# Optimization experiments

Measured on AMD Instinct MI355X. Metric: run time of the kernel, lower is better.

## Reference

```python
import jax, jax.numpy as jnp
import numpy as np

D_IN = 1024
D_OUT = 1024
SEQ = 4096


def setup_inputs() -> dict:
    key = jax.random.key(0)
    kx, kq, kk, kv = jax.random.split(key, 4)
    x = jax.random.normal(kx, (SEQ, D_IN), dtype=jnp.float32)
    # torch.rand -> uniform [0,1)
    wquery = jax.random.uniform(kq, (D_IN, D_OUT), dtype=jnp.float32)
    wkey = jax.random.uniform(kk, (D_IN, D_OUT), dtype=jnp.float32)
    wvalue = jax.random.uniform(kv, (D_IN, D_OUT), dtype=jnp.float32)
    return {"x": x, "wquery": wquery, "wkey": wkey, "wvalue": wvalue}


def reference(x, wquery, wkey, wvalue):
    keys = x @ wkey          # [S, d_out]
    queries = x @ wquery     # [S, d_out]
    values = x @ wvalue      # [S, d_out]
    scale = 1.0 / jnp.sqrt(jnp.float32(keys.shape[-1]))
    attn_scores = queries @ keys.T            # [S, S]
    attn_weights = jax.nn.softmax(attn_scores * scale, axis=-1)
    context = attn_weights @ values           # [S, d_out]
    return context
```

## Files before the change

kernel.cpp:

```cpp
#include <hip/hip_runtime.h>
#include <math.h>

#define SEQ 4096
#define DIM 1024

typedef _Float16 f16;
typedef _Float16 f16x8 __attribute__((ext_vector_type(8)));
typedef _Float16 f16x4 __attribute__((ext_vector_type(4)));
typedef float f32x4 __attribute__((ext_vector_type(4)));

#define GLOAD_LDS16(g, l)                                              \
    __builtin_amdgcn_global_load_lds(                                  \
        (const __attribute__((address_space(1))) void*)(g),            \
        (__attribute__((address_space(3))) void*)(l), 16, 0, 0)

__global__ __launch_bounds__(256) void split16(const float* __restrict__ in,
                                               f16* __restrict__ hi,
                                               f16* __restrict__ lo, int n4) {
    const int i = blockIdx.x * 256 + threadIdx.x;
    if (i >= n4) return;
    const float4 v = ((const float4*)in)[i];
    const float vv[4] = {v.x, v.y, v.z, v.w};
    f16x4 h, l;
#pragma unroll
    for (int q = 0; q < 4; ++q) {
        const f16 hq = (f16)vv[q];
        h[q] = hq;
        l[q] = (f16)(vv[q] - (float)hq);
    }
    ((f16x4*)hi)[i] = h;
    ((f16x4*)lo)[i] = l;
}

__global__ __launch_bounds__(256) void wtrans3h(
    const float* __restrict__ Wq, const float* __restrict__ Wk,
    const float* __restrict__ Wv,
    f16* __restrict__ QT, f16* __restrict__ KT, f16* __restrict__ VT) {
    __shared__ float tile[32][33];
    const int tid = threadIdx.x;
    const int r0 = blockIdx.x * 32;
    const int c0 = blockIdx.y * 32;
    const int z = blockIdx.z;
    const float* W = (z == 0) ? Wq : (z == 1) ? Wk : Wv;
    f16* T = (z == 0) ? QT : (z == 1) ? KT : VT;
    const float off = (z < 2) ? 0.5f : 0.0f;
    {
        const int r = tid >> 3, c = (tid & 7) * 4;
        const float4 v = *(const float4*)&W[(size_t)(r0 + r) * DIM + c0 + c];
        tile[r][c + 0] = v.x;
        tile[r][c + 1] = v.y;
        tile[r][c + 2] = v.z;
        tile[r][c + 3] = v.w;
    }
    __syncthreads();
    {
        const int n = tid >> 3;
        const int k = (tid & 7) * 4;
        f16x4 h;
#pragma unroll
        for (int q = 0; q < 4; ++q) h[q] = (f16)(tile[k + q][n] - off);
        *(f16x4*)&T[(size_t)(c0 + n) * DIM + r0 + k] = h;
    }
}

__global__ __launch_bounds__(256) void rowsum_x(const float* __restrict__ X,
                                                float* __restrict__ sx) {
    const int row = blockIdx.x * 4 + (threadIdx.x >> 6);
    const int lane = threadIdx.x & 63;
    const float4* r4 = (const float4*)(X + (size_t)row * DIM);
    float s = 0.f;
#pragma unroll
    for (int c = 0; c < 4; ++c) {
        const float4 f = r4[lane + 64 * c];
        s += f.x + f.y + f.z + f.w;
    }
#pragma unroll
    for (int m = 32; m >= 1; m >>= 1) s += __shfl_xor(s, m);
    if (lane == 0) sx[row] = s;
}

__global__ __launch_bounds__(256) void rowsum_hl(
    const f16* __restrict__ Qh, const f16* __restrict__ Ql,
    const f16* __restrict__ Kh, const f16* __restrict__ Kl,
    float* __restrict__ rq, float* __restrict__ rk) {
    const f16 *H, *L;
    float* out;
    if (blockIdx.y == 0) { H = Qh; L = Ql; out = rq; }
    else                 { H = Kh; L = Kl; out = rk; }
    const int row = blockIdx.x * 4 + (threadIdx.x >> 6);
    const int lane = threadIdx.x & 63;
    const f16x8* h8 = (const f16x8*)(H + (size_t)row * DIM);
    const f16x8* l8 = (const f16x8*)(L + (size_t)row * DIM);
    float s = 0.f;
#pragma unroll
    for (int c = 0; c < 2; ++c) {
        const f16x8 a = h8[lane + 64 * c];
        const f16x8 b = l8[lane + 64 * c];
#pragma unroll
        for (int e = 0; e < 8; ++e) s += (float)a[e] + (float)b[e];
    }
#pragma unroll
    for (int m = 32; m >= 1; m >>= 1) s += __shfl_xor(s, m);
    if (lane == 0) out[row] = s;
}

#define EPI_F32 0
#define EPI_SPLIT16 1
#define EPI_TRANS16 2

template <int EPI, int NPAIR, int KTILES>
__global__ __launch_bounds__(256, 2) void gemm128h(
    const f16* __restrict__ A0, const f16* __restrict__ A1,
    const f16* __restrict__ B0a, const f16* __restrict__ B1a,
    const f16* __restrict__ B0b, const f16* __restrict__ B1b,
    int ysplit, int N, int ldA, int ldB, float scale,
    void* out0a, void* out1a, void* out0b, void* out1b) {
    __shared__ __align__(16) f16 As[2][128 * 64];
    __shared__ __align__(16) f16 Bs[2][128 * 64];

    const int tid = threadIdx.x;
    const int lane = tid & 63;
    const int wid = tid >> 6;
    const int wr = wid >> 1, wc = wid & 1;

    const int total = (int)(gridDim.y << 5);
    int lid = (int)blockIdx.y * 32 + (int)blockIdx.x;
    lid = (lid & 7) * (total >> 3) + (lid >> 3);
    const int bx = lid & 31;
    int by = lid >> 5;

    const f16 *B0, *B1;
    void *o0, *o1;
    if (by >= ysplit) {
        by -= ysplit;
        B0 = B0b; B1 = B1b;
        o0 = out0b; o1 = out1b;
    } else {
        B0 = B0a; B1 = B1a;
        o0 = out0a; o1 = out1a;
    }
    const int m0 = bx * 128;
    const int n0 = by * 128;

    const f16* APs[2] = {A0, A1};
    const f16* BPs[2] = {B0, B1};
    const int nt = NPAIR * KTILES;

    f32x4 acc[4][4];
#pragma unroll
    for (int i = 0; i < 4; ++i)
#pragma unroll
        for (int j = 0; j < 4; ++j) acc[i][j] = (f32x4){0.f, 0.f, 0.f, 0.f};

    auto STAGE = [&](int t, int b) {
        const int pass = t / KTILES;
        const int k0 = (t % KTILES) * 64;
        const f16* Ap = APs[pass];
        const f16* Bp = BPs[pass];
#pragma unroll
        for (int L = 0; L < 4; ++L) {
            const int idx = L * 256 + tid;
            const int row = idx >> 3;
            const int sc = ((idx & 7) * 16) ^ ((row & 7) << 4);
            const int ldsu = (L * 256 + (tid & ~63)) * 8;
            GLOAD_LDS16(Ap + (size_t)(m0 + row) * ldA + k0 + (sc >> 1),
                        &As[b][ldsu]);
            GLOAD_LDS16(Bp + (size_t)(n0 + row) * ldB + k0 + (sc >> 1),
                        &Bs[b][ldsu]);
        }
    };

    STAGE(0, 0);

    for (int t = 0; t < nt; ++t) {
        const int cur = t & 1;
        __builtin_amdgcn_s_barrier();
        asm volatile("" ::: "memory");
        if (t + 1 < nt) {
            STAGE(t + 1, cur ^ 1);
            asm volatile("s_waitcnt vmcnt(8)" ::: "memory");
        } else {
            asm volatile("s_waitcnt vmcnt(0)" ::: "memory");
        }
        __builtin_amdgcn_s_barrier();
        asm volatile("" ::: "memory");

#pragma unroll
        for (int kk = 0; kk < 2; ++kk) {
            const int cb = kk * 64 + (lane >> 4) * 16;
            f16x8 af[4], bv[4];
#pragma unroll
            for (int i = 0; i < 4; ++i) {
                const int r = wr * 64 + i * 16 + (lane & 15);
                af[i] = *(const f16x8*)(&As[cur][r * 64 +
                                                 ((cb ^ ((r & 7) << 4)) >> 1)]);
            }
#pragma unroll
            for (int j = 0; j < 4; ++j) {
                const int r = wc * 64 + j * 16 + (lane & 15);
                bv[j] = *(const f16x8*)(&Bs[cur][r * 64 +
                                                 ((cb ^ ((r & 7) << 4)) >> 1)]);
            }
            __builtin_amdgcn_s_setprio(1);
#pragma unroll
            for (int i = 0; i < 4; ++i)
#pragma unroll
                for (int j = 0; j < 4; ++j)
                    acc[i][j] = __builtin_amdgcn_mfma_f32_16x16x32_f16(
                        af[i], bv[j], acc[i][j], 0, 0, 0);
            __builtin_amdgcn_s_setprio(0);
        }
    }

    const int row0 = m0 + wr * 64 + (lane >> 4) * 4;
    const int col0 = n0 + wc * 64 + (lane & 15);

    if (EPI == EPI_F32) {
        float* O = (float*)o0;
#pragma unroll
        for (int i = 0; i < 4; ++i)
#pragma unroll
            for (int j = 0; j < 4; ++j)
#pragma unroll
                for (int q = 0; q < 4; ++q)
                    O[(size_t)(row0 + i * 16 + q) * N + col0 + j * 16] =
                        acc[i][j][q] * scale;
    } else if (EPI == EPI_SPLIT16) {
        f16* Hi = (f16*)o0;
        f16* Lo = (f16*)o1;
#pragma unroll
        for (int i = 0; i < 4; ++i)
#pragma unroll
            for (int j = 0; j < 4; ++j)
#pragma unroll
                for (int q = 0; q < 4; ++q) {
                    const float x = acc[i][j][q];
                    const f16 h = (f16)x;
                    const size_t idx = (size_t)(row0 + i * 16 + q) * N + col0 + j * 16;
                    Hi[idx] = h;
                    Lo[idx] = (f16)(x - (float)h);
                }
    } else {
        f16* OT = (f16*)o0;
#pragma unroll
        for (int i = 0; i < 4; ++i)
#pragma unroll
            for (int j = 0; j < 4; ++j) {
                f16x4 v;
#pragma unroll
                for (int q = 0; q < 4; ++q) v[q] = (f16)acc[i][j][q];
                *(f16x4*)&OT[(size_t)(col0 + j * 16) * SEQ + row0 + i * 16] = v;
            }
    }
}

template <int NPAIR, int KT>
__global__ __launch_bounds__(512, 2) void qkrank1(
    const f16* __restrict__ A0, const f16* __restrict__ B0,
    const f16* __restrict__ A1, const f16* __restrict__ B1,
    const float* __restrict__ sx, const float* __restrict__ rq,
    const float* __restrict__ rk,
    int N, float scale, float* __restrict__ out) {
    constexpr int K = KT * 64;
    constexpr int nt = NPAIR * KT;
    __shared__ __align__(16) f16 As[2][256 * 64];
    __shared__ __align__(16) f16 Bs[2][256 * 64];

    const int tid = threadIdx.x;
    const int lane = tid & 63;
    const int wid = tid >> 6;
    const int wr = wid >> 2;
    const int wc = wid & 3;

    const int wg = ((int)blockIdx.x & 7) * 32 + ((int)blockIdx.x >> 3);
    const int m0 = (wg >> 4) * 256;
    const int n0 = (wg & 15) * 256;

    const f16* APs[2] = {A0, A1};
    const f16* BPs[2] = {B0, B1};

    f32x4 acc[8][4];
#pragma unroll
    for (int i = 0; i < 8; ++i)
#pragma unroll
        for (int j = 0; j < 4; ++j) acc[i][j] = (f32x4){0.f, 0.f, 0.f, 0.f};

    auto STAGE = [&](int t, int b) {
        const f16* Ap = APs[t / KT];
        const f16* Bp = BPs[t / KT];
        const int k0 = (t % KT) * 64;
#pragma unroll
        for (int L = 0; L < 4; ++L) {
            const int idx = L * 512 + tid;
            const int row = idx >> 3;
            const int sc = ((idx & 7) * 16) ^ ((row & 7) << 4);
            const int ldsu = (L * 512 + (tid & ~63)) * 8;
            GLOAD_LDS16(Ap + (size_t)(m0 + row) * K + k0 + (sc >> 1),
                        &As[b][ldsu]);
            GLOAD_LDS16(Bp + (size_t)(n0 + row) * K + k0 + (sc >> 1),
                        &Bs[b][ldsu]);
        }
    };

    STAGE(0, 0);

    for (int t = 0; t < nt; ++t) {
        const int cur = t & 1;
        __builtin_amdgcn_s_barrier();
        asm volatile("" ::: "memory");
        if (t + 1 < nt) {
            STAGE(t + 1, cur ^ 1);
            asm volatile("s_waitcnt vmcnt(8)" ::: "memory");
        } else {
            asm volatile("s_waitcnt vmcnt(0)" ::: "memory");
        }
        __builtin_amdgcn_s_barrier();
        asm volatile("" ::: "memory");

#pragma unroll
        for (int kk = 0; kk < 2; ++kk) {
            const int cb = kk * 64 + (lane >> 4) * 16;
            f16x8 af[8], bv[4];
#pragma unroll
            for (int i = 0; i < 8; ++i) {
                const int r = wr * 128 + i * 16 + (lane & 15);
                af[i] = *(const f16x8*)(&As[cur][r * 64 +
                                                 ((cb ^ ((r & 7) << 4)) >> 1)]);
            }
#pragma unroll
            for (int j = 0; j < 4; ++j) {
                const int r = wc * 64 + j * 16 + (lane & 15);
                bv[j] = *(const f16x8*)(&Bs[cur][r * 64 +
                                                 ((cb ^ ((r & 7) << 4)) >> 1)]);
            }
            __builtin_amdgcn_s_setprio(1);
#pragma unroll
            for (int i = 0; i < 8; ++i)
#pragma unroll
                for (int j = 0; j < 4; ++j)
                    acc[i][j] = __builtin_amdgcn_mfma_f32_16x16x32_f16(
                        af[i], bv[j], acc[i][j], 0, 0, 0);
            __builtin_amdgcn_s_setprio(0);
        }
    }

    const int row0 = m0 + wr * 128 + (lane >> 4) * 4;
    const int col0 = n0 + wc * 64 + (lane & 15);
    float u[4], w4[4];
#pragma unroll
    for (int j = 0; j < 4; ++j) {
        const float sxc = sx[col0 + j * 16];
        u[j] = 256.f * sxc + 0.5f * rk[col0 + j * 16];
        w4[j] = 0.5f * sxc;
    }
#pragma unroll
    for (int i = 0; i < 8; ++i)
#pragma unroll
        for (int q = 0; q < 4; ++q) {
            const int r = row0 + i * 16 + q;
            const float sxr = sx[r];
            const float rqr = rq[r];
#pragma unroll
            for (int j = 0; j < 4; ++j)
                out[(size_t)r * N + col0 + j * 16] =
                    (acc[i][j][q] + sxr * u[j] + rqr * w4[j]) * scale;
        }
}

__global__ __launch_bounds__(256) void softmax16(float* __restrict__ S) {
    __shared__ float red[8];
    const int tid = threadIdx.x;
    const size_t row = blockIdx.x;
    const float4* s4 = (const float4*)(S + row * SEQ);

    float4 v[4];
    float mx = -1e30f;
#pragma unroll
    for (int c = 0; c < 4; ++c) {
        v[c] = s4[c * 256 + tid];
        mx = fmaxf(mx, fmaxf(fmaxf(v[c].x, v[c].y), fmaxf(v[c].z, v[c].w)));
    }
#pragma unroll
    for (int m = 32; m >= 1; m >>= 1) mx = fmaxf(mx, __shfl_xor(mx, m));
    if ((tid & 63) == 0) red[tid >> 6] = mx;
    __syncthreads();
    mx = fmaxf(fmaxf(red[0], red[1]), fmaxf(red[2], red[3]));

    float e[16];
    float sum = 0.f;
#pragma unroll
    for (int c = 0; c < 4; ++c) {
        e[c * 4 + 0] = __expf(v[c].x - mx);
        e[c * 4 + 1] = __expf(v[c].y - mx);
        e[c * 4 + 2] = __expf(v[c].z - mx);
        e[c * 4 + 3] = __expf(v[c].w - mx);
        sum += e[c * 4] + e[c * 4 + 1] + e[c * 4 + 2] + e[c * 4 + 3];
    }
#pragma unroll
    for (int m = 32; m >= 1; m >>= 1) sum += __shfl_xor(sum, m);
    if ((tid & 63) == 0) red[4 + (tid >> 6)] = sum;
    __syncthreads();
    sum = red[4] + red[5] + red[6] + red[7];
    const float inv = 1.f / sum;

    f16* prow = (f16*)(S + row * SEQ);
#pragma unroll
    for (int c = 0; c < 4; ++c) {
        f16x4 o;
#pragma unroll
        for (int q = 0; q < 4; ++q) o[q] = (f16)(e[c * 4 + q] * inv);
        ((f16x4*)prow)[c * 256 + tid] = o;
    }
}

extern "C" void kernel_launch(void* const* d_in, const int* in_sizes, int n_in,
                              void* d_out, int out_size, void* d_ws, size_t ws_size,
                              hipStream_t stream) {
    const float* x  = (const float*)d_in[0];
    const float* wq = (const float*)d_in[1];
    const float* wk = (const float*)d_in[2];
    const float* wv = (const float*)d_in[3];
    float* O = (float*)d_out;

    char* ws = (char*)d_ws;
    const size_t MB = 1024 * 1024;
    const size_t KB = 1024;
    f16* Qh = (f16*)(ws + 0 * MB);
    f16* Ql = (f16*)(ws + 8 * MB);
    f16* Kh = (f16*)(ws + 16 * MB);
    f16* VT = (f16*)(ws + 24 * MB);
    float* sx = (float*)(ws + 32 * MB);
    float* rq = (float*)(ws + 32 * MB + 16 * KB);
    float* rk = (float*)(ws + 32 * MB + 32 * KB);
    float* S  = (float*)(ws + 40 * MB);
    f16* Xh  = (f16*)(ws + 40 * MB);
    f16* Xl  = (f16*)(ws + 48 * MB);
    f16* Wqh = (f16*)(ws + 56 * MB);
    f16* Wkh = (f16*)(ws + 58 * MB);
    f16* Wvh = (f16*)(ws + 60 * MB);
    f16* Kl  = (f16*)(ws + 64 * MB);

    split16<<<4096, 256, 0, stream>>>(x, Xh, Xl, SEQ * DIM / 4);
    wtrans3h<<<dim3(DIM / 32, DIM / 32, 3), 256, 0, stream>>>(
        wq, wk, wv, Wqh, Wkh, Wvh);
    rowsum_x<<<1024, 256, 0, stream>>>(x, sx);

    gemm128h<EPI_SPLIT16, 2, 16><<<dim3(32, 16), 256, 0, stream>>>(
        Xh, Xl, Wqh, Wqh, Wkh, Wkh,
        8, DIM, DIM, DIM, 1.f, Qh, Ql, Kh, Kl);

    rowsum_hl<<<dim3(1024, 2), 256, 0, stream>>>(Qh, Ql, Kh, Kl, rq, rk);

    gemm128h<EPI_TRANS16, 1, 16><<<dim3(32, 8), 256, 0, stream>>>(
        Xh, Xh, Wvh, Wvh, Wvh, Wvh,
        8, DIM, DIM, DIM, 1.f, VT, nullptr, VT, nullptr);

    qkrank1<2, 16><<<256, 512, 0, stream>>>(
        Qh, Kh, Ql, Kh, sx, rq, rk, SEQ, 0.03125f, S);

    softmax16<<<SEQ, 256, 0, stream>>>(S);

    gemm128h<EPI_F32, 1, 64><<<dim3(32, 8), 256, 0, stream>>>(
        (const f16*)S, (const f16*)S, VT, VT, VT, VT,
        8, DIM, 2 * SEQ, SEQ, 1.f, O, nullptr, O, nullptr);
}
```

Baseline: 236.9 us.

## Fuse partial softmax into QK GEMM epilogue and fold row sums into split

The QK score kernel now computes per-block row maxima and exponential sums in its epilogue and writes unnormalized fp16 probabilities instead of fp32 scores. A light rowfix kernel then rescales each row using the 16 block-wise max/sum partials. This drops the 64MB fp32 score write and the full softmax read pass, and the PV GEMM now reads a dense fp16 matrix with a plain stride. Separately, the x row sums are computed inside the split kernel, which removes the rowsum_x launch. In exchange the epilogue gains extra shuffles, LDS traffic and syncs, and probabilities are stored in fp16 before the final scaling.

Measured after the change: 235.2 us. Within noise of the previous version (-0.7%).

```diff
diff --git a/kernel.cpp b/kernel.cpp
--- a/kernel.cpp
+++ b/kernel.cpp
@@ -14,11 +14,13 @@
         (const __attribute__((address_space(1))) void*)(g),            \
         (__attribute__((address_space(3))) void*)(l), 16, 0, 0)
 
-__global__ __launch_bounds__(256) void split16(const float* __restrict__ in,
-                                               f16* __restrict__ hi,
-                                               f16* __restrict__ lo, int n4) {
-    const int i = blockIdx.x * 256 + threadIdx.x;
-    if (i >= n4) return;
+__global__ __launch_bounds__(256) void split16rs(const float* __restrict__ in,
+                                                 f16* __restrict__ hi,
+                                                 f16* __restrict__ lo,
+                                                 float* __restrict__ sx) {
+    __shared__ float sred[4];
+    const int tid = threadIdx.x;
+    const int i = blockIdx.x * 256 + tid;
     const float4 v = ((const float4*)in)[i];
     const float vv[4] = {v.x, v.y, v.z, v.w};
     f16x4 h, l;
@@ -30,6 +32,12 @@
     }
     ((f16x4*)hi)[i] = h;
     ((f16x4*)lo)[i] = l;
+    float s = v.x + v.y + v.z + v.w;
+#pragma unroll
+    for (int m = 32; m >= 1; m >>= 1) s += __shfl_xor(s, m);
+    if ((tid & 63) == 0) sred[tid >> 6] = s;
+    __syncthreads();
+    if (tid == 0) sx[blockIdx.x] = sred[0] + sred[1] + sred[2] + sred[3];
 }
 
 __global__ __launch_bounds__(256) void wtrans3h(
@@ -63,22 +71,6 @@
     }
 }
 
-__global__ __launch_bounds__(256) void rowsum_x(const float* __restrict__ X,
-                                                float* __restrict__ sx) {
-    const int row = blockIdx.x * 4 + (threadIdx.x >> 6);
-    const int lane = threadIdx.x & 63;
-    const float4* r4 = (const float4*)(X + (size_t)row * DIM);
-    float s = 0.f;
-#pragma unroll
-    for (int c = 0; c < 4; ++c) {
-        const float4 f = r4[lane + 64 * c];
-        s += f.x + f.y + f.z + f.w;
-    }
-#pragma unroll
-    for (int m = 32; m >= 1; m >>= 1) s += __shfl_xor(s, m);
-    if (lane == 0) sx[row] = s;
-}
-
 __global__ __launch_bounds__(256) void rowsum_hl(
     const f16* __restrict__ Qh, const f16* __restrict__ Ql,
     const f16* __restrict__ Kh, const f16* __restrict__ Kl,
@@ -260,7 +252,7 @@
     const f16* __restrict__ A1, const f16* __restrict__ B1,
     const float* __restrict__ sx, const float* __restrict__ rq,
     const float* __restrict__ rk,
-    int N, float scale, float* __restrict__ out) {
+    f16* __restrict__ Pu, float* __restrict__ Mp, float* __restrict__ Lp) {
     constexpr int K = KT * 64;
     constexpr int nt = NPAIR * KT;
     __shared__ __align__(16) f16 As[2][256 * 64];
@@ -275,6 +267,7 @@
     const int wg = ((int)blockIdx.x & 7) * 32 + ((int)blockIdx.x >> 3);
     const int m0 = (wg >> 4) * 256;
     const int n0 = (wg & 15) * 256;
+    const int bcol = n0 >> 8;
 
     const f16* APs[2] = {A0, A1};
     const f16* BPs[2] = {B0, B1};
@@ -344,8 +337,10 @@
         }
     }
 
-    const int row0 = m0 + wr * 128 + (lane >> 4) * 4;
-    const int col0 = n0 + wc * 64 + (lane & 15);
+    const int g4 = lane >> 4;
+    const int l15 = lane & 15;
+    const int row0 = m0 + wr * 128 + g4 * 4;
+    const int col0 = n0 + wc * 64 + l15;
     float u[4], w4[4];
 #pragma unroll
     for (int j = 0; j < 4; ++j) {
@@ -362,54 +357,112 @@
             const float rqr = rq[r];
 #pragma unroll
             for (int j = 0; j < 4; ++j)
-                out[(size_t)r * N + col0 + j * 16] =
-                    (acc[i][j][q] + sxr * u[j] + rqr * w4[j]) * scale;
-        }
-}
-
-__global__ __launch_bounds__(256) void softmax16(float* __restrict__ S) {
-    __shared__ float red[8];
+                acc[i][j][q] =
+                    (acc[i][j][q] + sxr * u[j] + rqr * w4[j]) * 0.03125f;
+        }
+
+    float* partm = (float*)&As[0][0];
+    float* mrow  = partm + 1024;
+    float* parts = mrow + 256;
+    float red[8][4];
+#pragma unroll
+    for (int i = 0; i < 8; ++i)
+#pragma unroll
+        for (int q = 0; q < 4; ++q) {
+            float v = acc[i][0][q];
+#pragma unroll
+            for (int j = 1; j < 4; ++j) v = fmaxf(v, acc[i][j][q]);
+            red[i][q] = v;
+        }
+#pragma unroll
+    for (int msk = 1; msk < 16; msk <<= 1)
+#pragma unroll
+        for (int i = 0; i < 8; ++i)
+#pragma unroll
+            for (int q = 0; q < 4; ++q)
+                red[i][q] = fmaxf(red[i][q], __shfl_xor(red[i][q], msk));
+    __syncthreads();
+    if (l15 == 0)
+#pragma unroll
+        for (int i = 0; i < 8; ++i)
+#pragma unroll
+            for (int q = 0; q < 4; ++q)
+                partm[(wr * 128 + i * 16 + g4 * 4 + q) * 4 + wc] = red[i][q];
+    __syncthreads();
+    if (tid < 256) {
+        const float* p = partm + tid * 4;
+        mrow[tid] = fmaxf(fmaxf(p[0], p[1]), fmaxf(p[2], p[3]));
+    }
+    __syncthreads();
+#pragma unroll
+    for (int i = 0; i < 8; ++i)
+#pragma unroll
+        for (int q = 0; q < 4; ++q) {
+            const float mB = mrow[wr * 128 + i * 16 + g4 * 4 + q];
+            float s = 0.f;
+#pragma unroll
+            for (int j = 0; j < 4; ++j) {
+                const float e = __expf(acc[i][j][q] - mB);
+                acc[i][j][q] = e;
+                s += e;
+            }
+            red[i][q] = s;
+        }
+#pragma unroll
+    for (int msk = 1; msk < 16; msk <<= 1)
+#pragma unroll
+        for (int i = 0; i < 8; ++i)
+#pragma unroll
+            for (int q = 0; q < 4; ++q) red[i][q] += __shfl_xor(red[i][q], msk);
+    if (l15 == 0)
+#pragma unroll
+        for (int i = 0; i < 8; ++i)
+#pragma unroll
+            for (int q = 0; q < 4; ++q)
+                parts[(wr * 128 + i * 16 + g4 * 4 + q) * 4 + wc] = red[i][q];
+    __syncthreads();
+    if (tid < 256) {
+        const float* p = parts + tid * 4;
+        Mp[(size_t)(m0 + tid) * 16 + bcol] = mrow[tid];
+        Lp[(size_t)(m0 + tid) * 16 + bcol] = p[0] + p[1] + p[2] + p[3];
+    }
+#pragma unroll
+    for (int i = 0; i < 8; ++i)
+#pragma unroll
+        for (int q = 0; q < 4; ++q) {
+            const size_t r = row0 + i * 16 + q;
+#pragma unroll
+            for (int j = 0; j < 4; ++j)
+                Pu[r * SEQ + col0 + j * 16] = (f16)acc[i][j][q];
+        }
+}
+
+__global__ __launch_bounds__(256) void rowfix(const float* __restrict__ Mp,
+                                              const float* __restrict__ Lp,
+                                              f16* __restrict__ Pu) {
+    __shared__ float mls[32];
     const int tid = threadIdx.x;
-    const size_t row = blockIdx.x;
-    const float4* s4 = (const float4*)(S + row * SEQ);
-
-    float4 v[4];
-    float mx = -1e30f;
-#pragma unroll
-    for (int c = 0; c < 4; ++c) {
-        v[c] = s4[c * 256 + tid];
-        mx = fmaxf(mx, fmaxf(fmaxf(v[c].x, v[c].y), fmaxf(v[c].z, v[c].w)));
-    }
-#pragma unroll
-    for (int m = 32; m >= 1; m >>= 1) mx = fmaxf(mx, __shfl_xor(mx, m));
-    if ((tid & 63) == 0) red[tid >> 6] = mx;
-    __syncthreads();
-    mx = fmaxf(fmaxf(red[0], red[1]), fmaxf(red[2], red[3]));
-
-    float e[16];
-    float sum = 0.f;
-#pragma unroll
-    for (int c = 0; c < 4; ++c) {
-        e[c * 4 + 0] = __expf(v[c].x - mx);
-        e[c * 4 + 1] = __expf(v[c].y - mx);
-        e[c * 4 + 2] = __expf(v[c].z - mx);
-        e[c * 4 + 3] = __expf(v[c].w - mx);
-        sum += e[c * 4] + e[c * 4 + 1] + e[c * 4 + 2] + e[c * 4 + 3];
-    }
-#pragma unroll
-    for (int m = 32; m >= 1; m >>= 1) sum += __shfl_xor(sum, m);
-    if ((tid & 63) == 0) red[4 + (tid >> 6)] = sum;
-    __syncthreads();
-    sum = red[4] + red[5] + red[6] + red[7];
-    const float inv = 1.f / sum;
-
-    f16* prow = (f16*)(S + row * SEQ);
-#pragma unroll
-    for (int c = 0; c < 4; ++c) {
-        f16x4 o;
-#pragma unroll
-        for (int q = 0; q < 4; ++q) o[q] = (f16)(e[c * 4 + q] * inv);
-        ((f16x4*)prow)[c * 256 + tid] = o;
+    const size_t r = blockIdx.x;
+    if (tid < 32)
+        mls[tid] = (tid < 16) ? Mp[r * 16 + tid] : Lp[r * 16 + tid - 16];
+    __syncthreads();
+    float m = -1e30f;
+#pragma unroll
+    for (int b = 0; b < 16; ++b) m = fmaxf(m, mls[b]);
+    float l = 0.f;
+#pragma unroll
+    for (int b = 0; b < 16; ++b) l += __expf(mls[b] - m) * mls[16 + b];
+    const float inv = 1.f / l;
+
+    f16* row = Pu + r * SEQ;
+#pragma unroll
+    for (int p = 0; p < 2; ++p) {
+        const int c0 = p * 2048 + tid * 8;
+        const float d = __expf(mls[c0 >> 8] - m) * inv;
+        f16x8 v = *(const f16x8*)(row + c0);
+#pragma unroll
+        for (int e = 0; e < 8; ++e) v[e] = (f16)((float)v[e] * d);
+        *(f16x8*)(row + c0) = v;
     }
 }
 
@@ -432,7 +485,9 @@
     float* sx = (float*)(ws + 32 * MB);
     float* rq = (float*)(ws + 32 * MB + 16 * KB);
     float* rk = (float*)(ws + 32 * MB + 32 * KB);
-    float* S  = (float*)(ws + 40 * MB);
+    float* Mp = (float*)(ws + 32 * MB + 48 * KB);
+    float* Lp = (float*)(ws + 32 * MB + 304 * KB);
+    f16* Pu = (f16*)(ws + 40 * MB);
     f16* Xh  = (f16*)(ws + 40 * MB);
     f16* Xl  = (f16*)(ws + 48 * MB);
     f16* Wqh = (f16*)(ws + 56 * MB);
@@ -440,10 +495,9 @@
     f16* Wvh = (f16*)(ws + 60 * MB);
     f16* Kl  = (f16*)(ws + 64 * MB);
 
-    split16<<<4096, 256, 0, stream>>>(x, Xh, Xl, SEQ * DIM / 4);
+    split16rs<<<4096, 256, 0, stream>>>(x, Xh, Xl, sx);
     wtrans3h<<<dim3(DIM / 32, DIM / 32, 3), 256, 0, stream>>>(
         wq, wk, wv, Wqh, Wkh, Wvh);
-    rowsum_x<<<1024, 256, 0, stream>>>(x, sx);
 
     gemm128h<EPI_SPLIT16, 2, 16><<<dim3(32, 16), 256, 0, stream>>>(
         Xh, Xl, Wqh, Wqh, Wkh, Wkh,
@@ -456,11 +510,11 @@
         8, DIM, DIM, DIM, 1.f, VT, nullptr, VT, nullptr);
 
     qkrank1<2, 16><<<256, 512, 0, stream>>>(
-        Qh, Kh, Ql, Kh, sx, rq, rk, SEQ, 0.03125f, S);
-
-    softmax16<<<SEQ, 256, 0, stream>>>(S);
+        Qh, Kh, Ql, Kh, sx, rq, rk, Pu, Mp, Lp);
+
+    rowfix<<<4096, 256, 0, stream>>>(Mp, Lp, Pu);
 
     gemm128h<EPI_F32, 1, 64><<<dim3(32, 8), 256, 0, stream>>>(
-        (const f16*)S, (const f16*)S, VT, VT, VT, VT,
-        8, DIM, 2 * SEQ, SEQ, 1.f, O, nullptr, O, nullptr);
-}
+        Pu, Pu, VT, VT, VT, VT,
+        8, DIM, SEQ, SEQ, 1.f, O, nullptr, O, nullptr);
+}
```
